# Kernel optimization log

Measured on AMD Instinct MI355X. Metric: run time of the kernel, lower is better.

## Reference

```python
import jax, jax.numpy as jnp
import numpy as np

B, S, D = 2, 1024, 4096
HQ, HKV, HD = 32, 8, 128
GROUPS = HQ // HKV          # 4
SCALE = HD ** -0.5


def _rope_tables(key):
    # standard RoPE cos/sin tables, non-interleaved (half-split) layout
    inv_freq = 1.0 / (10000.0 ** (jnp.arange(0, HD, 2, dtype=jnp.float32) / HD))  # [HD/2]
    pos = jnp.arange(S, dtype=jnp.float32)                                        # [S]
    freqs = pos[:, None] * inv_freq[None, :]                                      # [S, HD/2]
    emb = jnp.concatenate([freqs, freqs], axis=-1)                                # [S, HD]
    cos = jnp.broadcast_to(jnp.cos(emb)[None], (B, S, HD))
    sin = jnp.broadcast_to(jnp.sin(emb)[None], (B, S, HD))
    return cos, sin


def setup_inputs() -> dict:
    key = jax.random.key(0)
    ks = jax.random.split(key, 6)
    hidden_states = jax.random.normal(ks[0], (B, S, D), dtype=jnp.float32)
    cos_table, sin_table = _rope_tables(ks[1])
    Wq = jax.random.normal(ks[2], (D, HQ * HD), dtype=jnp.float32) * (D ** -0.5)
    Wk = jax.random.normal(ks[3], (D, HKV * HD), dtype=jnp.float32) * (D ** -0.5)
    Wv = jax.random.normal(ks[4], (D, HKV * HD), dtype=jnp.float32) * (D ** -0.5)
    Wo = jax.random.normal(ks[5], (HQ * HD, D), dtype=jnp.float32) * ((HQ * HD) ** -0.5)
    return {"hidden_states": hidden_states, "cos_table": cos_table,
            "sin_table": sin_table, "Wq": Wq, "Wk": Wk, "Wv": Wv, "Wo": Wo}


def _rotate_half(x):
    x1, x2 = jnp.split(x, 2, axis=-1)
    return jnp.concatenate([-x2, x1], axis=-1)


def _apply_rope(x, cos, sin):
    # x: [B, S, H, HD]; cos/sin: [B, S, HD] broadcast across heads
    c = cos[:, :, None, :]
    s = sin[:, :, None, :]
    return x * c + _rotate_half(x) * s


def reference(hidden_states, cos_table, sin_table, Wq, Wk, Wv, Wo):
    b, s, _ = hidden_states.shape
    # QKV projections (no bias, Llama-style)
    q = (hidden_states @ Wq).reshape(b, s, HQ, HD)
    k = (hidden_states @ Wk).reshape(b, s, HKV, HD)
    v = (hidden_states @ Wv).reshape(b, s, HKV, HD)
    # fused RoPE on q and k (in [B, S, H, HD] layout, as in source)
    q = _apply_rope(q, cos_table, sin_table)
    k = _apply_rope(k, cos_table, sin_table)
    # -> [B, H, S, HD]
    q = q.transpose(0, 2, 1, 3)
    k = k.transpose(0, 2, 1, 3)
    v = v.transpose(0, 2, 1, 3)
    # GQA repeat_kv: [B, HKV, S, HD] -> [B, HQ, S, HD]
    k = jnp.repeat(k, GROUPS, axis=1)
    v = jnp.repeat(v, GROUPS, axis=1)
    # SDPA, no mask (source calls sdpa without a mask)
    scores = jnp.einsum('bhqd,bhkd->bhqk', q, k) * SCALE
    attn = jax.nn.softmax(scores, axis=-1)
    out = jnp.einsum('bhqk,bhkd->bhqd', attn, v)
    out = out.transpose(0, 2, 1, 3).reshape(b, s, HQ * HD)
    return out @ Wo
```

## Files before the change

### kernel.cpp

```cpp
#include <hip/hip_runtime.h>

#define B_   2
#define S_   1024
#define D_   4096
#define HQ_  32
#define HKV_ 8
#define HD_  128
#define SCALE_ 0.08838834764831845f

typedef unsigned short u16;
typedef __attribute__((ext_vector_type(8))) short s16x8;
typedef __attribute__((ext_vector_type(4))) short s16x4;
typedef __attribute__((ext_vector_type(4))) float f32x4;

#define MFMA(a,b,c) __builtin_amdgcn_mfma_f32_16x16x32_bf16((a),(b),(c),0,0,0)

__device__ __forceinline__ u16 bf16_rne(float x) {
  unsigned u = __float_as_uint(x);
  u += 0x7fffu + ((u >> 16) & 1u);
  return (u16)(u >> 16);
}
__device__ __forceinline__ float bf16_up(u16 h) {
  return __uint_as_float(((unsigned)h) << 16);
}
__device__ __forceinline__ void split2(float x, u16& h, u16& l) {
  h = bf16_rne(x);
  l = bf16_rne(x - bf16_up(h));
}

__device__ __forceinline__ void cvt_hi_lo(float a, float b, unsigned& hi, unsigned& lo) {
  unsigned h, l;
  asm("v_cvt_pk_bf16_f32 %0, %1, %2" : "=v"(h) : "v"(a), "v"(b));
  float ra = __uint_as_float(h << 16);
  float rb = __uint_as_float(h & 0xffff0000u);
  float la = a - ra, lb = b - rb;
  asm("v_cvt_pk_bf16_f32 %0, %1, %2" : "=v"(l) : "v"(la), "v"(lb));
  hi = h; lo = l;
}
__device__ __forceinline__ void pack8(float4 x, float4 y, uint4& h, uint4& l) {
  unsigned h0,h1,h2,h3,l0,l1,l2,l3;
  cvt_hi_lo(x.x, x.y, h0, l0);
  cvt_hi_lo(x.z, x.w, h1, l1);
  cvt_hi_lo(y.x, y.y, h2, l2);
  cvt_hi_lo(y.z, y.w, h3, l3);
  h = make_uint4(h0,h1,h2,h3); l = make_uint4(l0,l1,l2,l3);
}

typedef const __attribute__((address_space(1))) void* gas_ptr;
typedef __attribute__((address_space(3))) void* las_ptr;
__device__ __forceinline__ void gload_lds16(const void* g, void* l) {
  __builtin_amdgcn_global_load_lds((gas_ptr)g, (las_ptr)l, 16, 0, 0);
}

__global__ __launch_bounds__(256) void frag_b2(
    const float* __restrict__ W, u16* __restrict__ dh, u16* __restrict__ dl,
    int N, int n0, int Ntot16, int ntoff)
{
  __shared__ float T[32][68];
  const int kt = blockIdx.x, nbk = blockIdx.y;
  const int tid = threadIdx.x;
#pragma unroll
  for (int rep = 0; rep < 2; ++rep) {
    int idx = tid + rep * 256;
    int row = idx >> 4, c4 = (idx & 15) * 4;
    float4 v = *reinterpret_cast<const float4*>(&W[(size_t)(kt*32 + row) * N + n0 + nbk*64 + c4]);
    *reinterpret_cast<float4*>(&T[row][c4]) = v;
  }
  __syncthreads();
  int c = tid;
  int nt = c >> 6, l = c & 63;
  const size_t base = (((size_t)(kt >> 1) * Ntot16 + ntoff + nbk*4 + nt) * 2 + (kt & 1)) * 512;
  u16 hh[8], ll[8];
#pragma unroll
  for (int j = 0; j < 8; ++j) split2(T[(l >> 4)*8 + j][nt*16 + (l & 15)], hh[j], ll[j]);
  *reinterpret_cast<s16x8*>(&dh[base + (size_t)l * 8]) =
    (s16x8){(short)hh[0],(short)hh[1],(short)hh[2],(short)hh[3],
            (short)hh[4],(short)hh[5],(short)hh[6],(short)hh[7]};
  *reinterpret_cast<s16x8*>(&dl[base + (size_t)l * 8]) =
    (s16x8){(short)ll[0],(short)ll[1],(short)ll[2],(short)ll[3],
            (short)ll[4],(short)ll[5],(short)ll[6],(short)ll[7]};
}

__global__ __launch_bounds__(256) void frag_a(
    const float* __restrict__ src, u16* __restrict__ dh, u16* __restrict__ dl)
{
  __shared__ float T[128][68];
  const int kt = blockIdx.x;
  const int mb = blockIdx.y;
  const int tid = threadIdx.x;
#pragma unroll
  for (int rep = 0; rep < 8; ++rep) {
    int idx = tid + rep * 256;
    int row = idx >> 4, c4 = (idx & 15) * 4;
    float4 v = *reinterpret_cast<const float4*>(&src[(size_t)(mb*128 + row) * 4096 + kt*64 + c4]);
    *reinterpret_cast<float4*>(&T[row][c4]) = v;
  }
  __syncthreads();
#pragma unroll
  for (int rep = 0; rep < 4; ++rep) {
    int c = tid + rep * 256;
    int mt = c >> 7, rem = c & 127, kk = rem >> 6, l = rem & 63;
    u16 hh[8], ll[8];
#pragma unroll
    for (int j = 0; j < 8; ++j)
      split2(T[mt*16 + (l & 15)][kk*32 + (l >> 4)*8 + j], hh[j], ll[j]);
    size_t off = (((size_t)(kt*128 + mb*8 + mt)) * 2 + kk) * 512 + (size_t)l * 8;
    *reinterpret_cast<s16x8*>(&dh[off]) =
      (s16x8){(short)hh[0],(short)hh[1],(short)hh[2],(short)hh[3],
              (short)hh[4],(short)hh[5],(short)hh[6],(short)hh[7]};
    *reinterpret_cast<s16x8*>(&dl[off]) =
      (s16x8){(short)ll[0],(short)ll[1],(short)ll[2],(short)ll[3],
              (short)ll[4],(short)ll[5],(short)ll[6],(short)ll[7]};
  }
}

template<int NF, bool RQ>
__device__ __forceinline__ void gemm256_core(
    const u16* __restrict__ PAh, const u16* __restrict__ PAl,
    const u16* __restrict__ PBh, const u16* __restrict__ PBl,
    float* __restrict__ C0, float* __restrict__ C1, float* __restrict__ C2,
    int ldc0, int Nt16, int mb, int nb, int vk0, int nvk, u16* L)
{
  const int tid  = threadIdx.x;
  const int lane = tid & 63;
  const int wid  = tid >> 6;
  const int loff = lane * 8;
  const int wm8  = (wid >> 2) * 8;
  const int wnf  = (wid & 3) * NF;

  u16* A0 = L;
  u16* A1 = L + 16384;
  u16* B0 = L + 32768;
  u16* B1 = L + 32768 + NF*4096;

  f32x4 acc[8][NF];
#pragma unroll
  for (int i = 0; i < 8; ++i)
#pragma unroll
    for (int j = 0; j < NF; ++j) acc[i][j] = (f32x4){0.f,0.f,0.f,0.f};

  const size_t aBase = (size_t)mb * 16384;
  const size_t bBase = (size_t)nb * (NF * 4096);
  const size_t bSlab = (size_t)Nt16 * 1024;

  auto STAGE = [&](int v, u16* la_, u16* lb_) {
    int p = v >> 6, k = v & 63;
    const u16* sa = ((p == 1) ? PAl : PAh) + (size_t)k * 131072 + aBase + loff;
    const u16* sb = ((p == 2) ? PBl : PBh) + (size_t)k * bSlab + bBase + loff;
#pragma unroll
    for (int s = 0; s < 4; ++s)
      gload_lds16(sa + (wid*4 + s)*512, la_ + (wid*4 + s)*512);
#pragma unroll
    for (int s = 0; s < NF; ++s)
      gload_lds16(sb + (wid*NF + s)*512, lb_ + (wid*NF + s)*512);
  };

  STAGE(vk0, (vk0 & 1) ? A1 : A0, (vk0 & 1) ? B1 : B0);
  __syncthreads();

  for (int t = vk0; t < vk0 + nvk; ++t) {
    u16* la = (t & 1) ? A1 : A0;
    u16* lb = (t & 1) ? B1 : B0;
    if (t + 1 < vk0 + nvk)
      STAGE(t + 1, (t & 1) ? A0 : A1, (t & 1) ? B0 : B1);
#pragma unroll
    for (int kk = 0; kk < 2; ++kk) {
      s16x8 a[8];
#pragma unroll
      for (int mf = 0; mf < 8; ++mf)
        a[mf] = *reinterpret_cast<const s16x8*>(&la[((wm8+mf)*2 + kk)*512 + loff]);
      __builtin_amdgcn_s_setprio(1);
#pragma unroll
      for (int nf = 0; nf < NF; ++nf) {
        s16x8 b = *reinterpret_cast<const s16x8*>(&lb[((wnf+nf)*2 + kk)*512 + loff]);
#pragma unroll
        for (int mf = 0; mf < 8; ++mf)
          acc[mf][nf] = MFMA(a[mf], b, acc[mf][nf]);
      }
      __builtin_amdgcn_s_setprio(0);
    }
    __syncthreads();
  }

  const int lg = lane >> 4, lr = lane & 15;
  const int rowb = mb*256 + (wid >> 2) * 128;
#pragma unroll
  for (int mf = 0; mf < 8; ++mf)
#pragma unroll
    for (int nf = 0; nf < NF; ++nf)
#pragma unroll
      for (int r = 0; r < 4; ++r) {
        int row = rowb + mf*16 + lg*4 + r;
        float v = acc[mf][nf][r];
        if constexpr (RQ) {
          int gcol = nb*(NF*64) + (wid & 3)*(NF*16) + nf*16 + lr;
          if (gcol < 4096)      C0[(size_t)row * 4096 + gcol] = v;
          else if (gcol < 5120) C1[(size_t)row * 1024 + (gcol - 4096)] = v;
          else                  C2[(size_t)row * 1024 + (gcol - 5120)] = v;
        } else {
          int col = nb*(NF*64) + (wid & 3)*(NF*16) + nf*16 + lr;
          C0[(size_t)row * ldc0 + col] = v;
        }
      }
}

__global__ __launch_bounds__(512) void gemm_qkv3(
    const u16* __restrict__ XAh, const u16* __restrict__ XAl,
    const u16* __restrict__ WBh, const u16* __restrict__ WBl,
    float* __restrict__ qb, float* __restrict__ kb, float* __restrict__ vb)
{
  __shared__ __attribute__((aligned(16))) u16 L[57344];
  int id = blockIdx.x;
  int swz = (id & 7) * 32 + (id >> 3);
  int mb = swz >> 5, nb = swz & 31;
  gemm256_core<3, true>(XAh, XAl, WBh, WBl, qb, kb, vb, 0, 384, mb, nb, 0, 192, L);
}

__global__ __launch_bounds__(512) void gemm_qkv2(
    const u16* __restrict__ XAh, const u16* __restrict__ XAl,
    const u16* __restrict__ WA,
    float* __restrict__ qb, float* __restrict__ kb, float* __restrict__ vb)
{
  __shared__ __attribute__((aligned(16))) u16 L[65536];
  int id = blockIdx.x;
  int swz = (id & 7) * 24 + (id >> 3);
  const u16 *Bh, *Bl; float* C; int ldc, Nt16, mb, nb;
  if (swz < 128)      { Bh = WA;          Bl = WA+16777216; C = qb; ldc = 4096; Nt16 = 256; mb = swz & 7;  nb = swz >> 3; }
  else if (swz < 160) { int u = swz-128; Bh = WA+33554432; Bl = WA+37748736; C = kb; ldc = 1024; Nt16 = 64; mb = u & 7; nb = u >> 3; }
  else                { int u = swz-160; Bh = WA+41943040; Bl = WA+46137344; C = vb; ldc = 1024; Nt16 = 64; mb = u & 7; nb = u >> 3; }
  gemm256_core<4, false>(XAh, XAl, Bh, Bl, C, nullptr, nullptr, ldc, Nt16, mb, nb, 0, 192, L);
}

__global__ __launch_bounds__(512) void gemm_out2(
    const u16* __restrict__ ABh, const u16* __restrict__ ABl,
    const u16* __restrict__ WOh, const u16* __restrict__ WOl,
    float* __restrict__ outp, float* __restrict__ c2)
{
  __shared__ __attribute__((aligned(16))) u16 L[65536];
  int id = blockIdx.x;
  int swz = (id & 7) * 32 + (id >> 3);
  int u = swz & 127, s = swz >> 7;
  int mb = u & 7, nb = u >> 3;
  gemm256_core<4, false>(ABh, ABl, WOh, WOl, s ? c2 : outp, nullptr, nullptr,
                         4096, 256, mb, nb, s*96, 96, L);
}

__global__ __launch_bounds__(256) void add_out(
    float* __restrict__ o, const float* __restrict__ c2)
{
  int i = blockIdx.x * 256 + threadIdx.x;
  float4 a = reinterpret_cast<float4*>(o)[i];
  float4 b = reinterpret_cast<const float4*>(c2)[i];
  a.x += b.x; a.y += b.y; a.z += b.z; a.w += b.w;
  reinterpret_cast<float4*>(o)[i] = a;
}

__global__ __launch_bounds__(256) void frag_kv(
    const float* __restrict__ kb, const float* __restrict__ vb,
    const float* __restrict__ cosT, const float* __restrict__ sinT,
    u16* __restrict__ KFh, u16* __restrict__ KFl,
    u16* __restrict__ VFh, u16* __restrict__ VFl)
{
  __shared__ float T[32][132];
  const int bid  = blockIdx.x;
  const int isV  = bid >> 9;
  const int bkvh = (bid >> 5) & 15;
  const int chnk = bid & 31;
  const int tid  = threadIdx.x;
  const int b    = bkvh >> 3, kvh = bkvh & 7;

  const float* src = isV ? vb : kb;
  {
    int r0 = tid >> 5, c4 = (tid & 31) * 4;
    float sgn = (c4 < 64) ? -1.f : 1.f;
#pragma unroll
    for (int it = 0; it < 4; ++it) {
      int row = r0 + it * 8;
      int srow = chnk*32 + row;
      const float* rp = &src[(((size_t)(b * S_ + srow)) * HKV_ + kvh) * HD_];
      float4 v = *reinterpret_cast<const float4*>(rp + c4);
      if (!isV) {
        float4 p  = *reinterpret_cast<const float4*>(rp + (c4 ^ 64));
        float4 cc = *reinterpret_cast<const float4*>(&cosT[((size_t)(b*S_ + srow))*HD_ + c4]);
        float4 ss = *reinterpret_cast<const float4*>(&sinT[((size_t)(b*S_ + srow))*HD_ + c4]);
        v.x = v.x*cc.x + sgn*p.x*ss.x;
        v.y = v.y*cc.y + sgn*p.y*ss.y;
        v.z = v.z*cc.z + sgn*p.z*ss.z;
        v.w = v.w*cc.w + sgn*p.w*ss.w;
      }
      *reinterpret_cast<float4*>(&T[row][c4]) = v;
    }
  }
  __syncthreads();
#pragma unroll
  for (int rep = 0; rep < 2; ++rep) {
    int c2 = tid + rep * 256;
    int l = c2 & 63;
    u16 hh[8], ll[8];
    if (!isV) {
      int f = c2 >> 6, st_loc = f >> 2, dt = f & 3;
#pragma unroll
      for (int j = 0; j < 8; ++j)
        split2(T[st_loc*16 + (l & 15)][dt*32 + (l >> 4)*8 + j], hh[j], ll[j]);
      size_t off = ((size_t)bkvh*64 + chnk*2) * 2048 + (size_t)c2 * 8;
      *reinterpret_cast<s16x8*>(&KFh[off]) =
        (s16x8){(short)hh[0],(short)hh[1],(short)hh[2],(short)hh[3],
                (short)hh[4],(short)hh[5],(short)hh[6],(short)hh[7]};
      *reinterpret_cast<s16x8*>(&KFl[off]) =
        (s16x8){(short)ll[0],(short)ll[1],(short)ll[2],(short)ll[3],
                (short)ll[4],(short)ll[5],(short)ll[6],(short)ll[7]};
    } else {
      int dt16 = c2 >> 6;
#pragma unroll
      for (int j = 0; j < 8; ++j)
        split2(T[(l >> 4)*8 + j][dt16*16 + (l & 15)], hh[j], ll[j]);
      size_t off = ((size_t)bkvh*32 + chnk) * 4096 + (size_t)c2 * 8;
      *reinterpret_cast<s16x8*>(&VFh[off]) =
        (s16x8){(short)hh[0],(short)hh[1],(short)hh[2],(short)hh[3],
                (short)hh[4],(short)hh[5],(short)hh[6],(short)hh[7]};
      *reinterpret_cast<s16x8*>(&VFl[off]) =
        (s16x8){(short)ll[0],(short)ll[1],(short)ll[2],(short)ll[3],
                (short)ll[4],(short)ll[5],(short)ll[6],(short)ll[7]};
    }
  }
}

__global__ __launch_bounds__(512) void attn3(
    const float* __restrict__ qb,
    const float* __restrict__ cosT, const float* __restrict__ sinT,
    const u16* __restrict__ KFh, const u16* __restrict__ KFl,
    const u16* __restrict__ VFh, const u16* __restrict__ VFl,
    float* __restrict__ ob)
{
  __shared__ __attribute__((aligned(16))) u16 Klds[16384];
  __shared__ __attribute__((aligned(16))) u16 Vlds[16384];
  __shared__ u16 Ph[8][16][68], Pl[8][16][68];

  const int tid  = threadIdx.x;
  const int lane = tid & 63;
  const int wid  = tid >> 6;
  const int lr   = lane & 15;
  const int lg   = lane >> 4;
  const int loff = lane * 8;
  const int qt   = blockIdx.x;
  const int bh   = blockIdx.y;
  const int b    = bh >> 5, h = bh & 31;
  const int bkvh = b * 8 + (h >> 2);

  s16x8 qh[4], ql[4];
  {
    const int qrow = qt * 128 + wid * 16 + lr;
    const float* qp = qb + ((size_t)((b * S_ + qrow) * HQ_ + h)) * HD_;
    const float* cp = cosT + ((size_t)(b * S_ + qrow)) * HD_;
    const float* sp = sinT + ((size_t)(b * S_ + qrow)) * HD_;
#pragma unroll
    for (int kc = 0; kc < 4; ++kc) {
      const int d0 = kc * 32 + lg * 8;
      const float sgn = (d0 < 64) ? -1.f : 1.f;
      float4 v0 = *reinterpret_cast<const float4*>(qp + d0);
      float4 v1 = *reinterpret_cast<const float4*>(qp + d0 + 4);
      float4 p0 = *reinterpret_cast<const float4*>(qp + (d0 ^ 64));
      float4 p1 = *reinterpret_cast<const float4*>(qp + (d0 ^ 64) + 4);
      float4 c0 = *reinterpret_cast<const float4*>(cp + d0);
      float4 c1 = *reinterpret_cast<const float4*>(cp + d0 + 4);
      float4 s0 = *reinterpret_cast<const float4*>(sp + d0);
      float4 s1 = *reinterpret_cast<const float4*>(sp + d0 + 4);
      float4 r0, r1;
      r0.x = v0.x*c0.x + sgn*p0.x*s0.x;  r0.y = v0.y*c0.y + sgn*p0.y*s0.y;
      r0.z = v0.z*c0.z + sgn*p0.z*s0.z;  r0.w = v0.w*c0.w + sgn*p0.w*s0.w;
      r1.x = v1.x*c1.x + sgn*p1.x*s1.x;  r1.y = v1.y*c1.y + sgn*p1.y*s1.y;
      r1.z = v1.z*c1.z + sgn*p1.z*s1.z;  r1.w = v1.w*c1.w + sgn*p1.w*s1.w;
      uint4 h4, l4; pack8(r0, r1, h4, l4);
      qh[kc] = *reinterpret_cast<s16x8*>(&h4);
      ql[kc] = *reinterpret_cast<s16x8*>(&l4);
    }
  }

  f32x4 acc_o[8];
#pragma unroll
  for (int df = 0; df < 8; ++df) acc_o[df] = (f32x4){0.f, 0.f, 0.f, 0.f};
  float m_run[4] = {-1e30f, -1e30f, -1e30f, -1e30f};
  float l_run[4] = {0.f, 0.f, 0.f, 0.f};

  const u16* gKh = KFh + (size_t)bkvh * 131072;
  const u16* gKl = KFl + (size_t)bkvh * 131072;
  const u16* gVh = VFh + (size_t)bkvh * 131072;
  const u16* gVl = VFl + (size_t)bkvh * 131072;

#pragma unroll
  for (int i = 0; i < 4; ++i) {
    int idx = wid * 4 + i;
    const u16* src = (idx < 16) ? (gKh + idx*512) : (gKl + (idx-16)*512);
    u16* dst = Klds + ((idx < 16) ? idx*512 : 8192 + (idx-16)*512);
    gload_lds16(src + loff, dst);
  }
  __syncthreads();

  for (int t = 0; t < 16; ++t) {
#pragma unroll
    for (int i = 0; i < 4; ++i) {
      int idx = wid * 4 + i;
      const u16* src = (idx < 16) ? (gVh + t*8192 + idx*512)
                                  : (gVl + t*8192 + (idx-16)*512);
      u16* dst = Vlds + ((idx < 16) ? idx*512 : 8192 + (idx-16)*512);
      gload_lds16(src + loff, dst);
    }

    f32x4 accs[4];
#pragma unroll
    for (int nf = 0; nf < 4; ++nf) {
      accs[nf] = (f32x4){0.f, 0.f, 0.f, 0.f};
      s16x8 kh8[4], kl8[4];
#pragma unroll
      for (int kc = 0; kc < 4; ++kc) {
        kh8[kc] = *reinterpret_cast<const s16x8*>(&Klds[nf*2048 + kc*512 + loff]);
        kl8[kc] = *reinterpret_cast<const s16x8*>(&Klds[8192 + nf*2048 + kc*512 + loff]);
      }
#pragma unroll
      for (int kc = 0; kc < 4; ++kc) {
        accs[nf] = MFMA(qh[kc], kh8[kc], accs[nf]);
        accs[nf] = MFMA(ql[kc], kh8[kc], accs[nf]);
        accs[nf] = MFMA(qh[kc], kl8[kc], accs[nf]);
      }
    }
#pragma unroll
    for (int nf = 0; nf < 4; ++nf) accs[nf] *= SCALE_;

    float corr[4], rsum[4];
#pragma unroll
    for (int r = 0; r < 4; ++r) {
      float t0 = fmaxf(fmaxf(accs[0][r], accs[1][r]), fmaxf(accs[2][r], accs[3][r]));
      t0 = fmaxf(t0, __shfl_xor(t0, 1));
      t0 = fmaxf(t0, __shfl_xor(t0, 2));
      t0 = fmaxf(t0, __shfl_xor(t0, 4));
      t0 = fmaxf(t0, __shfl_xor(t0, 8));
      float mnew = fmaxf(m_run[r], t0);
      corr[r] = __expf(m_run[r] - mnew);
      m_run[r] = mnew;
      rsum[r] = 0.f;
    }
#pragma unroll
    for (int nf = 0; nf < 4; ++nf)
#pragma unroll
      for (int r = 0; r < 4; ++r) {
        float p = __expf(accs[nf][r] - m_run[r]);
        rsum[r] += p;
        u16 ph, pl;
        split2(p, ph, pl);
        Ph[wid][lg*4 + r][nf*16 + lr] = ph;
        Pl[wid][lg*4 + r][nf*16 + lr] = pl;
      }
#pragma unroll
    for (int r = 0; r < 4; ++r) {
      float s = rsum[r];
      s += __shfl_xor(s, 1); s += __shfl_xor(s, 2);
      s += __shfl_xor(s, 4); s += __shfl_xor(s, 8);
      l_run[r] = l_run[r] * corr[r] + s;
    }
#pragma unroll
    for (int df = 0; df < 8; ++df)
#pragma unroll
      for (int r = 0; r < 4; ++r) acc_o[df][r] *= corr[r];

    __syncthreads();

    if (t < 15) {
#pragma unroll
      for (int i = 0; i < 4; ++i) {
        int idx = wid * 4 + i;
        const u16* src = (idx < 16) ? (gKh + (t+1)*8192 + idx*512)
                                    : (gKl + (t+1)*8192 + (idx-16)*512);
        u16* dst = Klds + ((idx < 16) ? idx*512 : 8192 + (idx-16)*512);
        gload_lds16(src + loff, dst);
      }
    }

    s16x8 pa_h[2], pa_l[2];
#pragma unroll
    for (int kc = 0; kc < 2; ++kc) {
      pa_h[kc] = *reinterpret_cast<const s16x8*>(&Ph[wid][lr][kc*32 + lg*8]);
      pa_l[kc] = *reinterpret_cast<const s16x8*>(&Pl[wid][lr][kc*32 + lg*8]);
    }
#pragma unroll
    for (int df = 0; df < 8; ++df) {
      s16x8 vh8[2], vl8[2];
#pragma unroll
      for (int kc = 0; kc < 2; ++kc) {
        vh8[kc] = *reinterpret_cast<const s16x8*>(&Vlds[kc*4096 + df*512 + loff]);
        vl8[kc] = *reinterpret_cast<const s16x8*>(&Vlds[8192 + kc*4096 + df*512 + loff]);
      }
#pragma unroll
      for (int kc = 0; kc < 2; ++kc) {
        acc_o[df] = MFMA(pa_h[kc], vh8[kc], acc_o[df]);
        acc_o[df] = MFMA(pa_l[kc], vh8[kc], acc_o[df]);
        acc_o[df] = MFMA(pa_h[kc], vl8[kc], acc_o[df]);
      }
    }
    __syncthreads();
  }

  float inv_l[4];
#pragma unroll
  for (int r = 0; r < 4; ++r) inv_l[r] = 1.f / l_run[r];
#pragma unroll
  for (int df = 0; df < 8; ++df)
#pragma unroll
    for (int r = 0; r < 4; ++r) {
      int row = qt * 128 + wid * 16 + lg * 4 + r;
      ob[((size_t)((b * S_ + row) * HQ_ + h)) * HD_ + df*16 + lr] = acc_o[df][r] * inv_l[r];
    }
}

extern "C" void kernel_launch(void* const* d_in, const int* in_sizes, int n_in,
                              void* d_out, int out_size, void* d_ws, size_t ws_size,
                              hipStream_t stream)
{
  const float* hs   = (const float*)d_in[0];
  const float* cosT = (const float*)d_in[1];
  const float* sinT = (const float*)d_in[2];
  const float* Wq   = (const float*)d_in[3];
  const float* Wk   = (const float*)d_in[4];
  const float* Wv   = (const float*)d_in[5];
  const float* Wo   = (const float*)d_in[6];
  float* out = (float*)d_out;

  float* qb = (float*)d_ws;
  float* kb = qb + 8388608;
  float* vb = kb + 2097152;
  float* ab = vb + 2097152;
  u16*   FR = (u16*)(ab + 8388608);

  const size_t WS212 = 222298112ULL;
  const size_t WS208 = 218103808ULL;

  if (ws_size >= WS212) {
    u16* XAh = FR;
    u16* XAl = FR + 8388608;
    u16* WBh = FR + 16777216;
    u16* WBl = FR + 41943040;
    u16* KFh = FR + 16777216;
    u16* KFl = FR + 18874368;
    u16* VFh = FR + 20971520;
    u16* VFl = FR + 23068672;
    u16* WOh = FR + 25165824;
    u16* WOl = FR + 41943040;

    frag_a<<<dim3(64,16), 256, 0, stream>>>(hs, XAh, XAl);
    frag_b2<<<dim3(128,64), 256, 0, stream>>>(Wq, WBh, WBl, 4096, 0, 384, 0);
    frag_b2<<<dim3(128,16), 256, 0, stream>>>(Wk, WBh, WBl, 1024, 0, 384, 256);
    frag_b2<<<dim3(128,16), 256, 0, stream>>>(Wv, WBh, WBl, 1024, 0, 384, 320);
    gemm_qkv3<<<256, 512, 0, stream>>>(XAh, XAl, WBh, WBl, qb, kb, vb);
    frag_kv<<<1024, 256, 0, stream>>>(kb, vb, cosT, sinT, KFh, KFl, VFh, VFl);
    frag_b2<<<dim3(128,64), 256, 0, stream>>>(Wo, WOh, WOl, 4096, 0, 256, 0);
    attn3<<<dim3(8, 64), 512, 0, stream>>>(qb, cosT, sinT, KFh, KFl, VFh, VFl, ab);
    frag_a<<<dim3(64,16), 256, 0, stream>>>(ab, XAh, XAl);
    gemm_out2<<<256, 512, 0, stream>>>(XAh, XAl, WOh, WOl, out, qb);
    add_out<<<8192, 256, 0, stream>>>(out, qb);
  } else {
    u16* XAh = FR;
    u16* XAl = FR + 8388608;
    u16* WA  = FR + 16777216;
    frag_a<<<dim3(64,16), 256, 0, stream>>>(hs, XAh, XAl);
    frag_b2<<<dim3(128,64), 256, 0, stream>>>(Wq, WA,           WA+16777216, 4096, 0, 256, 0);
    frag_b2<<<dim3(128,16), 256, 0, stream>>>(Wk, WA+33554432,  WA+37748736, 1024, 0, 64, 0);
    frag_b2<<<dim3(128,16), 256, 0, stream>>>(Wv, WA+41943040,  WA+46137344, 1024, 0, 64, 0);
    gemm_qkv2<<<192, 512, 0, stream>>>(XAh, XAl, WA, qb, kb, vb);
    frag_kv<<<1024, 256, 0, stream>>>(kb, vb, cosT, sinT,
                                      WA, WA+2097152, WA+4194304, WA+6291456);
    frag_b2<<<dim3(128,64), 256, 0, stream>>>(Wo, WA+8388608, WA+25165824, 4096, 0, 256, 0);
    attn3<<<dim3(8, 64), 512, 0, stream>>>(qb, cosT, sinT,
                                           WA, WA+2097152, WA+4194304, WA+6291456, ab);
    frag_a<<<dim3(64,16), 256, 0, stream>>>(ab, XAh, XAl);
    gemm_out2<<<256, 512, 0, stream>>>(XAh, XAl, WA+8388608, WA+25165824, out, qb);
    add_out<<<8192, 256, 0, stream>>>(out, qb);
  }
}
```

Before: 690.5 us.

## Stage hi and lo bf16 splits together per K-step to reuse fragments

```diff
diff --git a/kernel.cpp b/kernel.cpp
--- a/kernel.cpp
+++ b/kernel.cpp
@@ -119,7 +119,7 @@
     const u16* __restrict__ PAh, const u16* __restrict__ PAl,
     const u16* __restrict__ PBh, const u16* __restrict__ PBl,
     float* __restrict__ C0, float* __restrict__ C1, float* __restrict__ C2,
-    int ldc0, int Nt16, int mb, int nb, int vk0, int nvk, u16* L)
+    int ldc0, int Nt16, int mb, int nb, int k0, int nk, u16* L)
 {
   const int tid  = threadIdx.x;
   const int lane = tid & 63;
@@ -139,46 +139,77 @@
 #pragma unroll
     for (int j = 0; j < NF; ++j) acc[i][j] = (f32x4){0.f,0.f,0.f,0.f};
 
-  const size_t aBase = (size_t)mb * 16384;
-  const size_t bBase = (size_t)nb * (NF * 4096);
-  const size_t bSlab = (size_t)Nt16 * 1024;
-
-  auto STAGE = [&](int v, u16* la_, u16* lb_) {
-    int p = v >> 6, k = v & 63;
-    const u16* sa = ((p == 1) ? PAl : PAh) + (size_t)k * 131072 + aBase + loff;
-    const u16* sb = ((p == 2) ? PBl : PBh) + (size_t)k * bSlab + bBase + loff;
-#pragma unroll
-    for (int s = 0; s < 4; ++s)
-      gload_lds16(sa + (wid*4 + s)*512, la_ + (wid*4 + s)*512);
-#pragma unroll
-    for (int s = 0; s < NF; ++s)
-      gload_lds16(sb + (wid*NF + s)*512, lb_ + (wid*NF + s)*512);
+  auto STAGE = [&](int t, u16* la_, u16* lb_) {
+    const int kt64 = t >> 1, kk = t & 1;
+    const size_t aSlab = (size_t)kt64 * 131072;
+    const size_t bSlab = (size_t)kt64 * ((size_t)Nt16 * 1024);
+    const int NCH = 32 + 8*NF;
+#pragma unroll
+    for (int c = wid; c < NCH; c += 8) {
+      const u16* src; u16* dst;
+      if (c < 16) {
+        src = PAh + aSlab + (((size_t)(mb*16 + c))*2 + kk)*512;
+        dst = la_ + c*512;
+      } else if (c < 32) {
+        int m = c - 16;
+        src = PAl + aSlab + (((size_t)(mb*16 + m))*2 + kk)*512;
+        dst = la_ + 8192 + m*512;
+      } else if (c < 32 + 4*NF) {
+        int n = c - 32;
+        src = PBh + bSlab + (((size_t)(nb*4*NF + n))*2 + kk)*512;
+        dst = lb_ + n*512;
+      } else {
+        int n = c - 32 - 4*NF;
+        src = PBl + bSlab + (((size_t)(nb*4*NF + n))*2 + kk)*512;
+        dst = lb_ + NF*2048 + n*512;
+      }
+      gload_lds16(src + loff, dst);
+    }
   };
 
-  STAGE(vk0, (vk0 & 1) ? A1 : A0, (vk0 & 1) ? B1 : B0);
+  STAGE(k0, (k0 & 1) ? A1 : A0, (k0 & 1) ? B1 : B0);
   __syncthreads();
 
-  for (int t = vk0; t < vk0 + nvk; ++t) {
+  for (int t = k0; t < k0 + nk; ++t) {
     u16* la = (t & 1) ? A1 : A0;
     u16* lb = (t & 1) ? B1 : B0;
-    if (t + 1 < vk0 + nvk)
+    if (t + 1 < k0 + nk)
       STAGE(t + 1, (t & 1) ? A0 : A1, (t & 1) ? B0 : B1);
-#pragma unroll
-    for (int kk = 0; kk < 2; ++kk) {
-      s16x8 a[8];
+
+    s16x8 ah[8], al[8], bh[NF], bl[NF];
+#pragma unroll
+    for (int mf = 0; mf < 8; ++mf)
+      ah[mf] = *reinterpret_cast<const s16x8*>(&la[(wm8+mf)*512 + loff]);
+#pragma unroll
+    for (int nf = 0; nf < NF; ++nf)
+      bh[nf] = *reinterpret_cast<const s16x8*>(&lb[(wnf+nf)*512 + loff]);
+    __builtin_amdgcn_s_setprio(1);
+#pragma unroll
+    for (int nf = 0; nf < NF; ++nf)
 #pragma unroll
       for (int mf = 0; mf < 8; ++mf)
-        a[mf] = *reinterpret_cast<const s16x8*>(&la[((wm8+mf)*2 + kk)*512 + loff]);
-      __builtin_amdgcn_s_setprio(1);
-#pragma unroll
-      for (int nf = 0; nf < NF; ++nf) {
-        s16x8 b = *reinterpret_cast<const s16x8*>(&lb[((wnf+nf)*2 + kk)*512 + loff]);
-#pragma unroll
-        for (int mf = 0; mf < 8; ++mf)
-          acc[mf][nf] = MFMA(a[mf], b, acc[mf][nf]);
-      }
-      __builtin_amdgcn_s_setprio(0);
-    }
+        acc[mf][nf] = MFMA(ah[mf], bh[nf], acc[mf][nf]);
+    __builtin_amdgcn_s_setprio(0);
+#pragma unroll
+    for (int mf = 0; mf < 8; ++mf)
+      al[mf] = *reinterpret_cast<const s16x8*>(&la[8192 + (wm8+mf)*512 + loff]);
+    __builtin_amdgcn_s_setprio(1);
+#pragma unroll
+    for (int nf = 0; nf < NF; ++nf)
+#pragma unroll
+      for (int mf = 0; mf < 8; ++mf)
+        acc[mf][nf] = MFMA(al[mf], bh[nf], acc[mf][nf]);
+    __builtin_amdgcn_s_setprio(0);
+#pragma unroll
+    for (int nf = 0; nf < NF; ++nf)
+      bl[nf] = *reinterpret_cast<const s16x8*>(&lb[NF*2048 + (wnf+nf)*512 + loff]);
+    __builtin_amdgcn_s_setprio(1);
+#pragma unroll
+    for (int nf = 0; nf < NF; ++nf)
+#pragma unroll
+      for (int mf = 0; mf < 8; ++mf)
+        acc[mf][nf] = MFMA(ah[mf], bl[nf], acc[mf][nf]);
+    __builtin_amdgcn_s_setprio(0);
     __syncthreads();
   }
 
@@ -213,7 +244,7 @@
   int id = blockIdx.x;
   int swz = (id & 7) * 32 + (id >> 3);
   int mb = swz >> 5, nb = swz & 31;
-  gemm256_core<3, true>(XAh, XAl, WBh, WBl, qb, kb, vb, 0, 384, mb, nb, 0, 192, L);
+  gemm256_core<3, true>(XAh, XAl, WBh, WBl, qb, kb, vb, 0, 384, mb, nb, 0, 128, L);
 }
 
 __global__ __launch_bounds__(512) void gemm_qkv2(
@@ -228,7 +259,7 @@
   if (swz < 128)      { Bh = WA;          Bl = WA+16777216; C = qb; ldc = 4096; Nt16 = 256; mb = swz & 7;  nb = swz >> 3; }
   else if (swz < 160) { int u = swz-128; Bh = WA+33554432; Bl = WA+37748736; C = kb; ldc = 1024; Nt16 = 64; mb = u & 7; nb = u >> 3; }
   else                { int u = swz-160; Bh = WA+41943040; Bl = WA+46137344; C = vb; ldc = 1024; Nt16 = 64; mb = u & 7; nb = u >> 3; }
-  gemm256_core<4, false>(XAh, XAl, Bh, Bl, C, nullptr, nullptr, ldc, Nt16, mb, nb, 0, 192, L);
+  gemm256_core<4, false>(XAh, XAl, Bh, Bl, C, nullptr, nullptr, ldc, Nt16, mb, nb, 0, 128, L);
 }
 
 __global__ __launch_bounds__(512) void gemm_out2(
@@ -242,7 +273,7 @@
   int u = swz & 127, s = swz >> 7;
   int mb = u & 7, nb = u >> 3;
   gemm256_core<4, false>(ABh, ABl, WOh, WOl, s ? c2 : outp, nullptr, nullptr,
-                         4096, 256, mb, nb, s*96, 96, L);
+                         4096, 256, mb, nb, s*64, 64, L);
 }
 
 __global__ __launch_bounds__(256) void add_out(
```

Measured after the change: 642.7 us. 6.9% less time.
